# Performance work log

Hardware: AMD Instinct MI355X
Metric: run time of the kernel (lower is better)

The kernel has to match this reference:

```python
import jax, jax.numpy as jnp
import numpy as np

B, DIM, HID = 16384, 1024, 2048


def _ln(x, g, b, eps=1e-5):
    m = x.mean(-1, keepdims=True)
    v = ((x - m) ** 2).mean(-1, keepdims=True)
    return (x - m) / jnp.sqrt(v + eps) * g + b


def _attn1(x_kv, Wv, bv, Wo, bo):
    # seq-len-1 MHA: softmax over a single key is exactly 1 (per head),
    # so output = out_proj(v_proj(kv)); q/k projections cancel identically.
    return (x_kv @ Wv.T + bv) @ Wo.T + bo


def _ffn(x, W1, b1, W2, b2):
    return jnp.maximum(x @ W1.T + b1, 0.0) @ W2.T + b2


def setup_inputs() -> dict:
    key = jax.random.key(0)
    ks = iter(jax.random.split(key, 32))
    s = 0.02
    d = {
        'visual_feat': jax.random.normal(next(ks), (B, DIM), jnp.float32),
        'text_feat': jax.random.normal(next(ks), (B, DIM), jnp.float32),
    }
    for tag in ('sv', 'st', 'v2t', 't2v'):
        d[f'Wv_{tag}'] = jax.random.normal(next(ks), (DIM, DIM), jnp.float32) * s
        d[f'bv_{tag}'] = jnp.zeros((DIM,), jnp.float32)
        d[f'Wo_{tag}'] = jax.random.normal(next(ks), (DIM, DIM), jnp.float32) * s
        d[f'bo_{tag}'] = jnp.zeros((DIM,), jnp.float32)
    for tag in ('v1', 't1', 'v2', 't2'):
        d[f'g_{tag}'] = jnp.ones((DIM,), jnp.float32)
        d[f'be_{tag}'] = jnp.zeros((DIM,), jnp.float32)
    for tag in ('v', 't'):
        d[f'W1_{tag}'] = jax.random.normal(next(ks), (HID, DIM), jnp.float32) * s
        d[f'b1_{tag}'] = jnp.zeros((HID,), jnp.float32)
        d[f'W2_{tag}'] = jax.random.normal(next(ks), (DIM, HID), jnp.float32) * s
        d[f'b2_{tag}'] = jnp.zeros((DIM,), jnp.float32)
    return d


def reference(visual_feat, text_feat,
              Wv_sv, bv_sv, Wo_sv, bo_sv,
              Wv_st, bv_st, Wo_st, bo_st,
              Wv_v2t, bv_v2t, Wo_v2t, bo_v2t,
              Wv_t2v, bv_t2v, Wo_t2v, bo_t2v,
              g_v1, be_v1, g_t1, be_t1, g_v2, be_v2, g_t2, be_t2,
              W1_v, b1_v, W2_v, b2_v, W1_t, b1_t, W2_t, b2_t):
    v_self = _ln(visual_feat + _attn1(visual_feat, Wv_sv, bv_sv, Wo_sv, bo_sv), g_v1, be_v1)
    t_self = _ln(text_feat + _attn1(text_feat, Wv_st, bv_st, Wo_st, bo_st), g_t1, be_t1)
    v_cross = _attn1(t_self, Wv_v2t, bv_v2t, Wo_v2t, bo_v2t)  # v queries t -> depends on kv=t_self only
    t_cross = _attn1(v_self, Wv_t2v, bv_t2v, Wo_t2v, bo_t2v)
    v_fused = _ln(visual_feat + (v_self + v_cross) * 0.5, g_v2, be_v2)
    t_fused = _ln(text_feat + (t_self + t_cross) * 0.5, g_t2, be_t2)
    v_out = v_fused + _ffn(v_fused, W1_v, b1_v, W2_v, b2_v)
    t_out = t_fused + _ffn(t_fused, W1_t, b1_t, W2_t, b2_t)
    new_context = (v_out + t_out) * 0.5
    return (v_out, t_out, new_context)
```

## Files before the change

kernel.cpp:

```cpp
#include <hip/hip_runtime.h>
#include <stdint.h>


typedef unsigned short u16;
typedef __bf16 bf16x8 __attribute__((ext_vector_type(8)));
typedef float f32x4 __attribute__((ext_vector_type(4)));

__device__ __forceinline__ u16 f2bf(float f) {
    uint32_t x = __float_as_uint(f);
    uint32_t r = (x + 0x7fffu + ((x >> 16) & 1u)) >> 16;
    return (u16)r;
}
__device__ __forceinline__ float bf2f(u16 u) {
    return __uint_as_float(((uint32_t)u) << 16);
}

__device__ __forceinline__ void glds16(const u16* g, u16* l) {
    __builtin_amdgcn_global_load_lds(
        (__attribute__((address_space(1))) void*)g,
        (__attribute__((address_space(3))) void*)l, 16, 0, 0);
}

struct Ptr4 { const float* p[4]; };
__global__ __launch_bounds__(256) void cvt4k(Ptr4 src, u16* __restrict__ dst,
                                             size_t zstride) {
    const int z = blockIdx.y;
    size_t i = ((size_t)blockIdx.x * 256 + threadIdx.x) * 4;
    float4 v = *(const float4*)&src.p[z][i];
    ushort4 o;
    o.x = f2bf(v.x); o.y = f2bf(v.y); o.z = f2bf(v.z); o.w = f2bf(v.w);
    *(ushort4*)&dst[z * zstride + i] = o;
}

__global__ __launch_bounds__(256) void tcvtk(Ptr4 src, u16* __restrict__ dst) {
    __shared__ float t[32][33];
    const int z = blockIdx.z;
    const float* s = src.p[z];
    const int bx = blockIdx.x * 32, by = blockIdx.y * 32;
    const int tx = threadIdx.x & 31, ty = threadIdx.x >> 5;
#pragma unroll
    for (int i = 0; i < 32; i += 8)
        t[ty + i][tx] = s[(size_t)(by + ty + i) * 1024 + bx + tx];
    __syncthreads();
    u16* d = dst + (size_t)z * (1024 * 1024);
#pragma unroll
    for (int i = 0; i < 32; i += 8)
        d[(size_t)(bx + ty + i) * 1024 + by + tx] = f2bf(t[tx][ty + i]);
}

struct BiasArgs { const float* Wo[4]; const float* bv[4]; const float* bo[4]; };
__global__ __launch_bounds__(256) void biask(BiasArgs a, float* __restrict__ out) {
    const int z = blockIdx.y;
    const int row = blockIdx.x * 4 + (threadIdx.x >> 6);
    const int lane = threadIdx.x & 63;
    const float* w = a.Wo[z] + (size_t)row * 1024 + lane * 16;
    const float* v = a.bv[z] + lane * 16;
    float s = 0.f;
#pragma unroll
    for (int i = 0; i < 16; i += 4) {
        float4 w4 = *(const float4*)&w[i];
        float4 v4 = *(const float4*)&v[i];
        s += w4.x * v4.x + w4.y * v4.y + w4.z * v4.z + w4.w * v4.w;
    }
#pragma unroll
    for (int o = 1; o < 64; o <<= 1) s += __shfl_xor(s, o);
    if (lane == 0) out[(size_t)z * 1024 + row] = s + a.bo[z][row];
}

__global__ __launch_bounds__(256) void copyb(const float* a, const float* b,
                                             const float* c, const float* d,
                                             float* __restrict__ o) {
    int i = blockIdx.x * 1024 + threadIdx.x * 4;
    float4 v;
    if (i < 2048)      v = *(const float4*)&a[i];
    else if (i < 4096) v = *(const float4*)&b[i - 2048];
    else if (i < 5120) v = *(const float4*)&c[i - 4096];
    else               v = *(const float4*)&d[i - 5120];
    *(float4*)&o[i] = v;
}

__global__ __launch_bounds__(256) void ctxk(const float* __restrict__ a,
                                            const float* __restrict__ b,
                                            float* __restrict__ o) {
    size_t i = ((size_t)blockIdx.x * 256 + threadIdx.x) * 4;
    float4 va = *(const float4*)&a[i];
    float4 vb = *(const float4*)&b[i];
    float4 vo;
    vo.x = 0.5f * (va.x + vb.x); vo.y = 0.5f * (va.y + vb.y);
    vo.z = 0.5f * (va.z + vb.z); vo.w = 0.5f * (va.w + vb.w);
    *(float4*)&o[i] = vo;
}

struct LnArgs {
    const float* x[2]; const u16* a1[2]; const u16* a2[2];
    const float* g[2]; const float* be[2]; u16* out[2]; float s;
};
__global__ __launch_bounds__(256) void ln2_kernel(LnArgs A) {
    const int y = blockIdx.y;
    const int tid = threadIdx.x;
    const size_t base = (size_t)blockIdx.x * 1024;
    const int i0 = tid * 4;

    float4 xv = *(const float4*)&A.x[y][base + i0];
    ushort4 u1 = *(const ushort4*)&A.a1[y][base + i0];
    float add[4] = {bf2f(u1.x), bf2f(u1.y), bf2f(u1.z), bf2f(u1.w)};
    if (A.a2[y]) {
        ushort4 u2 = *(const ushort4*)&A.a2[y][base + i0];
        add[0] += bf2f(u2.x); add[1] += bf2f(u2.y);
        add[2] += bf2f(u2.z); add[3] += bf2f(u2.w);
    }
    float v[4] = {xv.x, xv.y, xv.z, xv.w};
    float sum = 0.f, ss = 0.f;
#pragma unroll
    for (int j = 0; j < 4; ++j) {
        v[j] += A.s * add[j];
        sum += v[j];
        ss += v[j] * v[j];
    }
#pragma unroll
    for (int o = 1; o < 64; o <<= 1) {
        sum += __shfl_xor(sum, o);
        ss  += __shfl_xor(ss, o);
    }
    __shared__ float s1[4], s2[4];
    if ((tid & 63) == 0) { s1[tid >> 6] = sum; s2[tid >> 6] = ss; }
    __syncthreads();
    sum = s1[0] + s1[1] + s1[2] + s1[3];
    ss  = s2[0] + s2[1] + s2[2] + s2[3];
    const float mean = sum * (1.f / 1024.f);
    const float var  = ss * (1.f / 1024.f) - mean * mean;
    const float inv  = rsqrtf(var + 1e-5f);

    float4 gv = *(const float4*)&A.g[y][i0];
    float4 bv = *(const float4*)&A.be[y][i0];
    ushort4 o4;
    o4.x = f2bf((v[0] - mean) * inv * gv.x + bv.x);
    o4.y = f2bf((v[1] - mean) * inv * gv.y + bv.y);
    o4.z = f2bf((v[2] - mean) * inv * gv.z + bv.z);
    o4.w = f2bf((v[3] - mean) * inv * gv.w + bv.w);
    *(ushort4*)&A.out[y][base + i0] = o4;
}

#define GBAR()  asm volatile("s_barrier" ::: "memory")
#define LGKM0() asm volatile("s_waitcnt lgkmcnt(0)" ::: "memory")

__global__ __launch_bounds__(512, 2) void gemm256(
    const u16* __restrict__ A, const u16* __restrict__ W,
    const float* __restrict__ bias,
    int M, int N, int K, int mode,
    const u16* __restrict__ resid,
    u16* __restrict__ out_bf, float* __restrict__ out_f,
    size_t sA, size_t sW, size_t sC, size_t sB, size_t sR) {
    __shared__ u16 LDS[2][2][2][8192];

    const int tid  = threadIdx.x;
    const int lane = tid & 63;
    const int wv   = tid >> 6;
    const int wm   = wv >> 2, wn = wv & 3;

    const int gx   = gridDim.x;
    const int nwg  = gx * gridDim.y;
    const int orig = blockIdx.y * gx + blockIdx.x;
    const int qq = nwg >> 3, rr = nwg & 7;
    const int xcd = orig & 7, loc = orig >> 3;
    const int wgid =
        (xcd < rr ? xcd * (qq + 1) : rr * (qq + 1) + (xcd - rr) * qq) + loc;
    const int M0 = (wgid / gx) * 256, N0 = (wgid % gx) * 256;

    const int z = blockIdx.z;
    A += (size_t)z * sA;
    W += (size_t)z * sW;

    const f32x4 fz = {0.f, 0.f, 0.f, 0.f};
    f32x4 acc[8][4];
#pragma unroll
    for (int i = 0; i < 8; ++i)
#pragma unroll
        for (int j = 0; j < 4; ++j) acc[i][j] = fz;

    const int rl = lane >> 2;
    const int gS = (lane & 3) ^ ((lane >> 3) & 3);
    const u16* aS = A + (size_t)(M0 + wv * 32 + rl) * K + gS * 8;
    const u16* bS = W + (size_t)(N0 + wv * 32 + rl) * K + gS * 8;
    const size_t cstep = (size_t)16 * K;

    const int lr = lane & 15, qf = lane >> 4;
    const int fsw  = ((qf ^ ((lr >> 1) & 3)) << 3);
    const int arow = (wm * 128 + lr) * 32 + fsw;
    const int brow = (wn * 64 + lr) * 32 + fsw;

    const int nt = K >> 6;

    auto STAGE = [&](int mat, int t, int kh) {
        const u16* src = (mat ? bS : aS) + t * 64 + kh * 32;
        u16* dst = &LDS[t & 1][mat][kh][wv * 1024];
        glds16(src, dst);
        glds16(src + cstep, dst + 512);
    };

    STAGE(0, 0, 0); STAGE(0, 0, 1);
    STAGE(1, 0, 0); STAGE(1, 0, 1);
    if (nt > 1) {
        STAGE(1, 1, 0); STAGE(1, 1, 1);
        asm volatile("s_waitcnt vmcnt(4)" ::: "memory");
    } else {
        asm volatile("s_waitcnt vmcnt(0)" ::: "memory");
    }
    GBAR();

    for (int t = 0; t < nt; ++t) {
        const int b = t & 1;
        bf16x8 aF[4], bK[4];

#pragma unroll
        for (int mi = 0; mi < 4; ++mi)
            aF[mi] = *(const bf16x8*)&LDS[b][0][0][arow + mi * 512];
#pragma unroll
        for (int ni = 0; ni < 4; ++ni)
            bK[ni] = *(const bf16x8*)&LDS[b][1][0][brow + ni * 512];
        if (t + 1 < nt) STAGE(0, t + 1, 0);
        GBAR(); LGKM0();
        __builtin_amdgcn_s_setprio(1);
#pragma unroll
        for (int mi = 0; mi < 4; ++mi)
#pragma unroll
            for (int ni = 0; ni < 4; ++ni)
                acc[mi][ni] = __builtin_amdgcn_mfma_f32_16x16x32_bf16(
                    aF[mi], bK[ni], acc[mi][ni], 0, 0, 0);
        __builtin_amdgcn_s_setprio(0);
        GBAR();

#pragma unroll
        for (int mi = 0; mi < 4; ++mi)
            aF[mi] = *(const bf16x8*)&LDS[b][0][0][arow + (mi + 4) * 512];
        if (t + 1 < nt) STAGE(0, t + 1, 1);
        GBAR(); LGKM0();
        __builtin_amdgcn_s_setprio(1);
#pragma unroll
        for (int mi = 0; mi < 4; ++mi)
#pragma unroll
            for (int ni = 0; ni < 4; ++ni)
                acc[mi + 4][ni] = __builtin_amdgcn_mfma_f32_16x16x32_bf16(
                    aF[mi], bK[ni], acc[mi + 4][ni], 0, 0, 0);
        __builtin_amdgcn_s_setprio(0);
        GBAR();

#pragma unroll
        for (int mi = 0; mi < 4; ++mi)
            aF[mi] = *(const bf16x8*)&LDS[b][0][1][arow + mi * 512];
#pragma unroll
        for (int ni = 0; ni < 4; ++ni)
            bK[ni] = *(const bf16x8*)&LDS[b][1][1][brow + ni * 512];
        if (t + 2 < nt) STAGE(1, t + 2, 0);
        GBAR(); LGKM0();
        __builtin_amdgcn_s_setprio(1);
#pragma unroll
        for (int mi = 0; mi < 4; ++mi)
#pragma unroll
            for (int ni = 0; ni < 4; ++ni)
                acc[mi][ni] = __builtin_amdgcn_mfma_f32_16x16x32_bf16(
                    aF[mi], bK[ni], acc[mi][ni], 0, 0, 0);
        __builtin_amdgcn_s_setprio(0);
        GBAR();

#pragma unroll
        for (int mi = 0; mi < 4; ++mi)
            aF[mi] = *(const bf16x8*)&LDS[b][0][1][arow + (mi + 4) * 512];
        if (t + 2 < nt) STAGE(1, t + 2, 1);
        GBAR(); LGKM0();
        __builtin_amdgcn_s_setprio(1);
#pragma unroll
        for (int mi = 0; mi < 4; ++mi)
#pragma unroll
            for (int ni = 0; ni < 4; ++ni)
                acc[mi + 4][ni] = __builtin_amdgcn_mfma_f32_16x16x32_bf16(
                    aF[mi], bK[ni], acc[mi + 4][ni], 0, 0, 0);
        __builtin_amdgcn_s_setprio(0);
        if (t + 2 < nt) asm volatile("s_waitcnt vmcnt(4)" ::: "memory");
        else            asm volatile("s_waitcnt vmcnt(0)" ::: "memory");
        GBAR();
    }

    const int rb = M0 + wm * 128 + (qf << 2);
    const int cb = N0 + wn * 64 + lr;
    out_bf += (size_t)z * sC;
    out_f  += (size_t)z * sC;
    const float* bz = bias ? bias + (size_t)z * sB : nullptr;
    const u16* rz = resid ? resid + (size_t)z * sR : nullptr;
#pragma unroll
    for (int mi = 0; mi < 8; ++mi) {
#pragma unroll
        for (int ni = 0; ni < 4; ++ni) {
            const int c = cb + ni * 16;
            const float bv = bz ? bz[c] : 0.f;
#pragma unroll
            for (int r = 0; r < 4; ++r) {
                const int rrw = rb + mi * 16 + r;
                float val = acc[mi][ni][r] + bv;
                if (mode == 0) {
                    out_bf[(size_t)rrw * N + c] = f2bf(val);
                } else if (mode == 1) {
                    out_bf[(size_t)rrw * N + c] = f2bf(val > 0.f ? val : 0.f);
                } else {
                    out_f[(size_t)rrw * N + c] =
                        val + bf2f(rz[(size_t)rrw * N + c]);
                }
            }
        }
    }
}

extern "C" void kernel_launch(void* const* d_in, const int* in_sizes, int n_in,
                              void* d_out, int out_size, void* d_ws, size_t ws_size,
                              hipStream_t stream) {
    const float* visual = (const float*)d_in[0];
    const float* text   = (const float*)d_in[1];
    const float* Wv_sv  = (const float*)d_in[2];
    const float* bv_sv  = (const float*)d_in[3];
    const float* Wo_sv  = (const float*)d_in[4];
    const float* bo_sv  = (const float*)d_in[5];
    const float* Wv_st  = (const float*)d_in[6];
    const float* bv_st  = (const float*)d_in[7];
    const float* Wo_st  = (const float*)d_in[8];
    const float* bo_st  = (const float*)d_in[9];
    const float* Wv_v2t = (const float*)d_in[10];
    const float* bv_v2t = (const float*)d_in[11];
    const float* Wo_v2t = (const float*)d_in[12];
    const float* bo_v2t = (const float*)d_in[13];
    const float* Wv_t2v = (const float*)d_in[14];
    const float* bv_t2v = (const float*)d_in[15];
    const float* Wo_t2v = (const float*)d_in[16];
    const float* bo_t2v = (const float*)d_in[17];
    const float* g_v1 = (const float*)d_in[18];
    const float* be_v1 = (const float*)d_in[19];
    const float* g_t1 = (const float*)d_in[20];
    const float* be_t1 = (const float*)d_in[21];
    const float* g_v2 = (const float*)d_in[22];
    const float* be_v2 = (const float*)d_in[23];
    const float* g_t2 = (const float*)d_in[24];
    const float* be_t2 = (const float*)d_in[25];
    const float* W1_v = (const float*)d_in[26];
    const float* b1_v = (const float*)d_in[27];
    const float* W2_v = (const float*)d_in[28];
    const float* b2_v = (const float*)d_in[29];
    const float* W1_t = (const float*)d_in[30];
    const float* b1_t = (const float*)d_in[31];
    const float* W2_t = (const float*)d_in[32];
    const float* b2_t = (const float*)d_in[33];

    const int Bsz = 16384, D = 1024, HID = 2048;
    const size_t SQ = (size_t)D * D;
    const size_t BD = (size_t)Bsz * D;

    u16* wb = (u16*)d_ws;
    u16* wWc  = wb + 0 * SQ;
    u16* wW1  = wb + 4 * SQ;
    u16* wW2  = wb + 8 * SQ;
    float* bcAll = (float*)(wb + 12 * SQ);
    float* bF1   = bcAll + 4096;
    float* bF2   = bcAll + 8192;
    u16* XA = wb + 16 * SQ;
    u16* XS = wb + 48 * SQ;
    u16* XC = wb + 80 * SQ;
    u16* XF = wb + 112 * SQ;
    u16* H  = wb + 144 * SQ;
    u16* wWo  = wb + 208 * SQ;
    u16* wWvT = wb + 212 * SQ;

    float* out0 = (float*)d_out;
    float* out1 = out0 + BD;
    float* out2 = out0 + 2 * BD;

    auto gemm = [&](const u16* Am, const u16* Wm, const float* bias, int M,
                    int N, int K, int mode, const u16* resid, void* out,
                    int zdim, size_t sA, size_t sW, size_t sC, size_t sB,
                    size_t sR) {
        dim3 grid((unsigned)(N / 256), (unsigned)(M / 256), (unsigned)zdim);
        gemm256<<<grid, dim3(512), 0, stream>>>(Am, Wm, bias, M, N, K, mode,
                                                resid, (u16*)out, (float*)out,
                                                sA, sW, sC, sB, sR);
    };

    Ptr4 wop = {{Wo_sv, Wo_st, Wo_t2v, Wo_v2t}};
    cvt4k<<<dim3(1024, 4), dim3(256), 0, stream>>>(wop, wWo, SQ);
    Ptr4 wvp = {{Wv_sv, Wv_st, Wv_t2v, Wv_v2t}};
    tcvtk<<<dim3(32, 32, 4), dim3(256), 0, stream>>>(wvp, wWvT);
    Ptr4 w12 = {{W1_v, W1_t, W2_v, W2_t}};
    cvt4k<<<dim3(2048, 4), dim3(256), 0, stream>>>(w12, wW1, 2 * SQ);
    copyb<<<dim3(6), dim3(256), 0, stream>>>(b1_v, b1_t, b2_v, b2_t, bF1);

    gemm(wWo, wWvT, nullptr, D, D, D, 0, nullptr, wWc, 4, SQ, SQ, SQ, 0, 0);
    BiasArgs ba = {{Wo_sv, Wo_st, Wo_t2v, Wo_v2t},
                   {bv_sv, bv_st, bv_t2v, bv_v2t},
                   {bo_sv, bo_st, bo_t2v, bo_v2t}};
    biask<<<dim3(256, 4), dim3(256), 0, stream>>>(ba, bcAll);

    Ptr4 inp = {{visual, text, nullptr, nullptr}};
    cvt4k<<<dim3(16384, 2), dim3(256), 0, stream>>>(inp, XA, BD);

    gemm(XA, wWc, bcAll, Bsz, D, D, 0, nullptr, XS, 2, BD, SQ, BD, 1024, 0);
    {
        LnArgs la = {{visual, text}, {XS, XS + BD}, {nullptr, nullptr},
                     {g_v1, g_t1}, {be_v1, be_t1}, {XS, XS + BD}, 1.f};
        ln2_kernel<<<dim3(16384, 2), dim3(256), 0, stream>>>(la);
    }

    gemm(XS, wWc + 2 * SQ, bcAll + 2048, Bsz, D, D, 0, nullptr, XC, 2,
         BD, SQ, BD, 1024, 0);
    {
        LnArgs la = {{visual, text}, {XS, XS + BD}, {XC + BD, XC},
                     {g_v2, g_t2}, {be_v2, be_t2}, {XF, XF + BD}, 0.5f};
        ln2_kernel<<<dim3(16384, 2), dim3(256), 0, stream>>>(la);
    }

    gemm(XF, wW1, bF1, Bsz, HID, D, 1, nullptr, H, 2, BD, 2 * SQ, 2 * BD,
         2048, 0);
    gemm(H, wW2, bF2, Bsz, D, HID, 2, XF, out0, 2, 2 * BD, 2 * SQ, BD,
         1024, BD);

    ctxk<<<dim3((unsigned)(BD / 1024)), dim3(256), 0, stream>>>(out0, out1, out2);
}
```

Measured before the change: 1.115 ms.

## Switch GEMM main loop to triple-buffered 32-wide K stages with one barrier

```diff
diff --git a/kernel.cpp b/kernel.cpp
--- a/kernel.cpp
+++ b/kernel.cpp
@@ -142,7 +142,6 @@
 }
 
 #define GBAR()  asm volatile("s_barrier" ::: "memory")
-#define LGKM0() asm volatile("s_waitcnt lgkmcnt(0)" ::: "memory")
 
 __global__ __launch_bounds__(512, 2) void gemm256(
     const u16* __restrict__ A, const u16* __restrict__ W,
@@ -151,7 +150,7 @@
     const u16* __restrict__ resid,
     u16* __restrict__ out_bf, float* __restrict__ out_f,
     size_t sA, size_t sW, size_t sC, size_t sB, size_t sR) {
-    __shared__ u16 LDS[2][2][2][8192];
+    __shared__ u16 LDS[3][2][8192];
 
     const int tid  = threadIdx.x;
     const int lane = tid & 63;
@@ -189,19 +188,18 @@
     const int arow = (wm * 128 + lr) * 32 + fsw;
     const int brow = (wn * 64 + lr) * 32 + fsw;
 
-    const int nt = K >> 6;
-
-    auto STAGE = [&](int mat, int t, int kh) {
-        const u16* src = (mat ? bS : aS) + t * 64 + kh * 32;
-        u16* dst = &LDS[t & 1][mat][kh][wv * 1024];
+    const int nt = K >> 5;
+
+    auto STAGE = [&](int mat, int t) {
+        const u16* src = (mat ? bS : aS) + t * 32;
+        u16* dst = &LDS[t % 3][mat][wv * 1024];
         glds16(src, dst);
         glds16(src + cstep, dst + 512);
     };
 
-    STAGE(0, 0, 0); STAGE(0, 0, 1);
-    STAGE(1, 0, 0); STAGE(1, 0, 1);
+    STAGE(0, 0); STAGE(1, 0);
     if (nt > 1) {
-        STAGE(1, 1, 0); STAGE(1, 1, 1);
+        STAGE(0, 1); STAGE(1, 1);
         asm volatile("s_waitcnt vmcnt(4)" ::: "memory");
     } else {
         asm volatile("s_waitcnt vmcnt(0)" ::: "memory");
@@ -209,17 +207,16 @@
     GBAR();
 
     for (int t = 0; t < nt; ++t) {
-        const int b = t & 1;
-        bf16x8 aF[4], bK[4];
-
+        const int bu = t % 3;
+        bf16x8 aF[4], aG[4], bK[4];
+
+        if (t + 2 < nt) STAGE(0, t + 2);
 #pragma unroll
         for (int mi = 0; mi < 4; ++mi)
-            aF[mi] = *(const bf16x8*)&LDS[b][0][0][arow + mi * 512];
+            aF[mi] = *(const bf16x8*)&LDS[bu][0][arow + mi * 512];
 #pragma unroll
         for (int ni = 0; ni < 4; ++ni)
-            bK[ni] = *(const bf16x8*)&LDS[b][1][0][brow + ni * 512];
-        if (t + 1 < nt) STAGE(0, t + 1, 0);
-        GBAR(); LGKM0();
+            bK[ni] = *(const bf16x8*)&LDS[bu][1][brow + ni * 512];
         __builtin_amdgcn_s_setprio(1);
 #pragma unroll
         for (int mi = 0; mi < 4; ++mi)
@@ -228,54 +225,20 @@
                 acc[mi][ni] = __builtin_amdgcn_mfma_f32_16x16x32_bf16(
                     aF[mi], bK[ni], acc[mi][ni], 0, 0, 0);
         __builtin_amdgcn_s_setprio(0);
-        GBAR();
-
+
+        if (t + 2 < nt) STAGE(1, t + 2);
 #pragma unroll
         for (int mi = 0; mi < 4; ++mi)
-            aF[mi] = *(const bf16x8*)&LDS[b][0][0][arow + (mi + 4) * 512];
-        if (t + 1 < nt) STAGE(0, t + 1, 1);
-        GBAR(); LGKM0();
+            aG[mi] = *(const bf16x8*)&LDS[bu][0][arow + (mi + 4) * 512];
         __builtin_amdgcn_s_setprio(1);
 #pragma unroll
         for (int mi = 0; mi < 4; ++mi)
 #pragma unroll
             for (int ni = 0; ni < 4; ++ni)
                 acc[mi + 4][ni] = __builtin_amdgcn_mfma_f32_16x16x32_bf16(
-                    aF[mi], bK[ni], acc[mi + 4][ni], 0, 0, 0);
+                    aG[mi], bK[ni], acc[mi + 4][ni], 0, 0, 0);
         __builtin_amdgcn_s_setprio(0);
-        GBAR();
-
-#pragma unroll
-        for (int mi = 0; mi < 4; ++mi)
-            aF[mi] = *(const bf16x8*)&LDS[b][0][1][arow + mi * 512];
-#pragma unroll
-        for (int ni = 0; ni < 4; ++ni)
-            bK[ni] = *(const bf16x8*)&LDS[b][1][1][brow + ni * 512];
-        if (t + 2 < nt) STAGE(1, t + 2, 0);
-        GBAR(); LGKM0();
-        __builtin_amdgcn_s_setprio(1);
-#pragma unroll
-        for (int mi = 0; mi < 4; ++mi)
-#pragma unroll
-            for (int ni = 0; ni < 4; ++ni)
-                acc[mi][ni] = __builtin_amdgcn_mfma_f32_16x16x32_bf16(
-                    aF[mi], bK[ni], acc[mi][ni], 0, 0, 0);
-        __builtin_amdgcn_s_setprio(0);
-        GBAR();
-
-#pragma unroll
-        for (int mi = 0; mi < 4; ++mi)
-            aF[mi] = *(const bf16x8*)&LDS[b][0][1][arow + (mi + 4) * 512];
-        if (t + 2 < nt) STAGE(1, t + 2, 1);
-        GBAR(); LGKM0();
-        __builtin_amdgcn_s_setprio(1);
-#pragma unroll
-        for (int mi = 0; mi < 4; ++mi)
-#pragma unroll
-            for (int ni = 0; ni < 4; ++ni)
-                acc[mi + 4][ni] = __builtin_amdgcn_mfma_f32_16x16x32_bf16(
-                    aF[mi], bK[ni], acc[mi + 4][ni], 0, 0, 0);
-        __builtin_amdgcn_s_setprio(0);
+
         if (t + 2 < nt) asm volatile("s_waitcnt vmcnt(4)" ::: "memory");
         else            asm volatile("s_waitcnt vmcnt(0)" ::: "memory");
         GBAR();
```

New measurement: 1.127 ms. No clear change (+1.1%).
